# Kernel optimization log

Hardware: AMD Instinct MI355X
Metric: run time of the kernel (lower is better)

The kernel has to match this reference:

```python
import jax, jax.numpy as jnp
import numpy as np

FACTOR = 16
B = 65536
H = 50  # userids history length (mean-pooled)
# (name, vocab, factor_multiplier) in concat order of feature()
FEATS = [
    ("ip1", 256, 8), ("ip2", 256, 8), ("ip3", 256, 8),
    ("url", 2, 1), ("aurl", 2, 1),
    ("regionid", 35, 6), ("cityid", 370, 9), ("adexchange", 9, 4),
    ("adslotw", 21, 5), ("adsloth", 14, 4), ("adslotv", 7, 3),
    ("adslotfp", 275, 9), ("creativeid", 57, 6),
    ("bidprice", 2, 1), ("payprice", 295, 9), ("userids", 69, 7),
]


def setup_inputs() -> dict:
    key = jax.random.key(0)
    inp = {}
    for i, (name, vocab, mult) in enumerate(FEATS):
        k1, k2 = jax.random.split(jax.random.fold_in(key, i))
        shape = (B, H) if name == "userids" else (B,)
        inp["idx_" + name] = jax.random.randint(k1, shape, 0, vocab, dtype=jnp.int32)
        inp["E_" + name] = jax.random.normal(k2, (vocab, FACTOR * mult), dtype=jnp.float32) * 0.1
    dims = [FACTOR * 89, FACTOR * 64, FACTOR * 32, FACTOR * 16, 2]
    for i in range(4):
        k1, _ = jax.random.split(jax.random.fold_in(key, 100 + i))
        inp[f"W{i+1}"] = jax.random.normal(k1, (dims[i], dims[i + 1]), dtype=jnp.float32) * 0.02
        inp[f"b{i+1}"] = jnp.zeros((dims[i + 1],), dtype=jnp.float32)
    return inp


def reference(idx_ip1, idx_ip2, idx_ip3, idx_url, idx_aurl, idx_regionid,
              idx_cityid, idx_adexchange, idx_adslotw, idx_adsloth, idx_adslotv,
              idx_adslotfp, idx_creativeid, idx_bidprice, idx_payprice, idx_userids,
              E_ip1, E_ip2, E_ip3, E_url, E_aurl, E_regionid,
              E_cityid, E_adexchange, E_adslotw, E_adsloth, E_adslotv,
              E_adslotfp, E_creativeid, E_bidprice, E_payprice, E_userids,
              W1, b1, W2, b2, W3, b3, W4, b4):
    # 15 single-index gathers + mean-pooled userids, concatenated -> [B, factor*89]
    parts = [
        E_ip1[idx_ip1], E_ip2[idx_ip2], E_ip3[idx_ip3],
        E_url[idx_url], E_aurl[idx_aurl],
        E_regionid[idx_regionid], E_cityid[idx_cityid], E_adexchange[idx_adexchange],
        E_adslotw[idx_adslotw], E_adsloth[idx_adsloth], E_adslotv[idx_adslotv],
        E_adslotfp[idx_adslotfp], E_creativeid[idx_creativeid],
        E_bidprice[idx_bidprice], E_payprice[idx_payprice],
        E_userids[idx_userids].mean(axis=1),  # [B, H, d] -> [B, d]
    ]
    x = jnp.concatenate(parts, axis=-1)
    for W, b in ((W1, b1), (W2, b2), (W3, b3), (W4, b4)):
        x = jax.nn.relu(x @ W + b)  # ReLU after every layer, incl. last (as in source)
    return jax.nn.softmax(x, axis=-1)
```

## Files before the change

### kernel.cpp

```cpp
#include <hip/hip_runtime.h>
#include <stdint.h>

typedef unsigned short u16;
typedef __attribute__((ext_vector_type(8))) __bf16 bf16x8;
typedef __attribute__((ext_vector_type(4))) float f32x4;

#define B_TOTAL 65536
#define KPAD1   1440

__device__ __forceinline__ u16 f2bf(float f) {
  union { float f; uint32_t u; } v; v.f = f;
  uint32_t r = v.u + 0x7fffu + ((v.u >> 16) & 1u);
  return (u16)(r >> 16);
}

__device__ __forceinline__ void gload16(const void* g, void* lds) {
  __builtin_amdgcn_global_load_lds(
      (const __attribute__((address_space(1))) uint32_t*)g,
      (__attribute__((address_space(3))) uint32_t*)lds, 16, 0, 0);
}

constexpr int FDIM[15] = {128,128,128,16,16,96,144,64,80,64,48,144,96,16,144};
__device__ __constant__ int FOFF2[17] = {0,128,256,384,400,416,512,656,720,800,
                                         864,912,1056,1152,1168,1312,1440};
__device__ __constant__ int EOFF[15] = {0,32768,65536,98304,98336,98368,101728,
                                        155008,155584,157264,158160,158496,
                                        198096,203568,203600};
__device__ __constant__ int FDIMd[15] = {128,128,128,16,16,96,144,64,80,64,48,144,96,16,144};
#define EBF_TOTAL 246080

__global__ void wprep_kernel(const float* __restrict__ W, u16* __restrict__ Wt,
                             int K, int N, int Kpad) {
  int o = blockIdx.x * 256 + threadIdx.x;
  if (o >= N * Kpad) return;
  int k = o % Kpad;
  int n = o / Kpad;
  float v = (k < K) ? W[(size_t)k * N + n] : 0.0f;
  Wt[o] = f2bf(v);
}

struct EcvtArgs { const float* E[15]; };
__global__ void ecvt_kernel(EcvtArgs p, u16* __restrict__ ebf) {
  int i = blockIdx.x * 256 + threadIdx.x;
  if (i >= EBF_TOTAL) return;
  int f = 0;
#pragma unroll
  for (int t = 1; t < 15; ++t) if (i >= EOFF[t]) f = t;
  ebf[i] = f2bf(p.E[f][i - EOFF[f]]);
}

__global__ __launch_bounds__(512) void pool_kernel(const int* __restrict__ idx_u,
                                                   const float* __restrict__ E_u,
                                                   u16* __restrict__ P, int row_base) {
  __shared__ float eu_t[69 * 112];
  const int tid = threadIdx.x;
  {
    const float4* s4 = reinterpret_cast<const float4*>(E_u);
    float4* d4 = reinterpret_cast<float4*>(eu_t);
    for (int i = tid; i < 69 * 28; i += 512) d4[i] = s4[i];
  }
  const int lane = tid & 63;
  const int wv   = tid >> 6;
  const int row0 = blockIdx.x * 16 + wv * 2;

  const int* iu0 = idx_u + (size_t)(row_base + row0) * 50;
  const int myid0 = (lane < 50) ? iu0[lane] : 0;
  const int myid1 = (lane < 50) ? iu0[50 + lane] : 0;
  __syncthreads();

  const int half = lane >> 5;
  const int c    = lane & 31;

  auto POOL = [&](int myid, u16* prow) {
    float4 s = {0.f, 0.f, 0.f, 0.f};
    if (c < 28) {
      const float* eu = eu_t + c * 4;
      const int j0 = half * 25;
#pragma unroll
      for (int jb = 0; jb < 25; jb += 5) {
        float4 v0, v1, v2, v3, v4;
        {
          const int i0 = __shfl(myid, j0 + jb + 0);
          const int i1 = __shfl(myid, j0 + jb + 1);
          const int i2 = __shfl(myid, j0 + jb + 2);
          const int i3 = __shfl(myid, j0 + jb + 3);
          const int i4 = __shfl(myid, j0 + jb + 4);
          v0 = *reinterpret_cast<const float4*>(eu + i0 * 112);
          v1 = *reinterpret_cast<const float4*>(eu + i1 * 112);
          v2 = *reinterpret_cast<const float4*>(eu + i2 * 112);
          v3 = *reinterpret_cast<const float4*>(eu + i3 * 112);
          v4 = *reinterpret_cast<const float4*>(eu + i4 * 112);
        }
        s.x += v0.x + v1.x + v2.x + v3.x + v4.x;
        s.y += v0.y + v1.y + v2.y + v3.y + v4.y;
        s.z += v0.z + v1.z + v2.z + v3.z + v4.z;
        s.w += v0.w + v1.w + v2.w + v3.w + v4.w;
      }
      s.x += __shfl_xor(s.x, 32);
      s.y += __shfl_xor(s.y, 32);
      s.z += __shfl_xor(s.z, 32);
      s.w += __shfl_xor(s.w, 32);
      if (half == 0) {
        const float inv = 1.0f / 50.0f;
        ushort4 o;
        o.x = f2bf(s.x * inv);
        o.y = f2bf(s.y * inv);
        o.z = f2bf(s.z * inv);
        o.w = f2bf(s.w * inv);
        *reinterpret_cast<ushort4*>(prow + c * 4) = o;
      }
    } else if (half == 1) {
      ushort4 z; z.x = 0; z.y = 0; z.z = 0; z.w = 0;
      *reinterpret_cast<ushort4*>(prow + 112 + (c - 28) * 4) = z;
    }
  };

  POOL(myid0, P + (size_t)row0 * 128);
  POOL(myid1, P + (size_t)(row0 + 1) * 128);
}

#define TILE_ELE 16384

struct G1Args { const int* idx[15]; };

__global__ __launch_bounds__(512, 2) void gemm1g(
    G1Args p, const u16* __restrict__ ebf, const u16* __restrict__ P,
    const u16* __restrict__ Wt, const float* __restrict__ bias,
    u16* __restrict__ C, int N, int gm) {
  constexpr int K = KPAD1;
  constexpr int NT = K / 32;
  extern __shared__ __align__(16) u16 lds[];
  uint32_t* desc32 = reinterpret_cast<uint32_t*>(&lds[49152]);
  int* idxl = reinterpret_cast<int*>(&lds[49152 + 1440]);
  const int tid  = threadIdx.x;
  const int w    = tid >> 6;
  const int lane = tid & 63;
  const int fr   = lane & 15;
  const int kg   = lane >> 4;
  const int wm   = w >> 2;
  const int wn   = w & 3;

  const int nwg = gridDim.x;
  const int q = nwg >> 3, r = nwg & 7;
  const int xcd = blockIdx.x & 7, lid = blockIdx.x >> 3;
  const int swz = (xcd < r) ? (xcd * (q + 1) + lid) : (r * (q + 1) + (xcd - r) * q + lid);
  const int gn = N >> 8;
  const int bn = swz % gn, bm = swz / gn;
  const int rowBase = bm * 256, colBase = bn * 256;

  if (tid < 180) {
    const int c0 = tid * 8;
    int f = 0;
#pragma unroll
    for (int t = 1; t < 16; ++t) if (c0 >= FOFF2[t]) f = t;
    const u16* base = (f < 15) ? (ebf + EOFF[f]) : P;
    const int dim = (f < 15) ? FDIMd[f] : 128;
    const int off = c0 - FOFF2[f];
    desc32[tid * 4 + 0] = (uint32_t)(uintptr_t)base;
    desc32[tid * 4 + 1] = (uint32_t)((uintptr_t)base >> 32);
    desc32[tid * 4 + 2] = (uint32_t)dim;
    desc32[tid * 4 + 3] = (uint32_t)(off | (f << 16));
  }
#pragma unroll
  for (int f = 0; f < 15; ++f)
    if (tid < 256) idxl[tid * 17 + f] = p.idx[f][rowBase + tid];
  if (tid < 256) idxl[tid * 17 + 15] = tid;
  __syncthreads();

  const int srow  = lane >> 2;
  const int sslot = (lane & 3) ^ ((lane >> 3) & 3);
  const u16* Bsrc0 = Wt + (size_t)(colBase + w * 16 + srow) * K + sslot * 8;
  const size_t rstep = (size_t)128 * K;
  const int r0 = w * 16 + srow;

  f32x4 acc[8][4];
#pragma unroll
  for (int m = 0; m < 8; ++m)
#pragma unroll
    for (int n = 0; n < 4; ++n)
      acc[m][n] = f32x4{0.f, 0.f, 0.f, 0.f};

  const int aslot8 = (kg ^ ((fr >> 1) & 3)) * 8;
  const int ardA = (wm * 128 + fr) * 32 + aslot8;
  const int ardB = (wn * 64 + fr) * 32 + aslot8 + 8192;

  auto stageA = [&](int ldsElemBase, int kt) {
    const int g = kt * 4 + sslot;
    const uint32_t d0 = desc32[g * 4 + 0];
    const uint32_t d1 = desc32[g * 4 + 1];
    const uint32_t d2 = desc32[g * 4 + 2];
    const uint32_t d3 = desc32[g * 4 + 3];
    const u16* base = (const u16*)(((uint64_t)d1 << 32) | (uint64_t)d0);
    const int dim = (int)d2;
    const int off = (int)(d3 & 0xffffu);
    const int fid = (int)(d3 >> 16);
    const int i0 = idxl[r0 * 17 + fid];
    const int i1 = idxl[(r0 + 128) * 17 + fid];
    gload16(base + (size_t)i0 * dim + off, &lds[ldsElemBase + w * 512]);
    gload16(base + (size_t)i1 * dim + off, &lds[ldsElemBase + w * 512 + 4096]);
  };
  auto stageB = [&](int ldsElemBase, int kt) {
    const u16* s = Bsrc0 + (size_t)kt * 32;
    gload16(s,         &lds[ldsElemBase + w * 512]);
    gload16(s + rstep, &lds[ldsElemBase + w * 512 + 4096]);
  };

  stageA(0 * TILE_ELE,        0);
  stageB(0 * TILE_ELE + 8192, 0);
  stageA(1 * TILE_ELE,        1);
  stageB(1 * TILE_ELE + 8192, 1);

  for (int t = 0; t < NT; ++t) {
    const int cb = t % 3;
    const int sb = (t + 2) % 3;
    const bool dost = (t + 2) < NT;
    const int cA = cb * TILE_ELE;

    __builtin_amdgcn_sched_barrier(0);
    if (t < NT - 1) asm volatile("s_waitcnt vmcnt(4)" ::: "memory");
    else            asm volatile("s_waitcnt vmcnt(0)" ::: "memory");
    __builtin_amdgcn_s_barrier();
    __builtin_amdgcn_sched_barrier(0);

    if (dost) {
      stageA(sb * TILE_ELE,        t + 2);
      stageB(sb * TILE_ELE + 8192, t + 2);
    }

    bf16x8 a0 = *(const bf16x8*)&lds[cA + ardA + 0 * 512];
    bf16x8 a1 = *(const bf16x8*)&lds[cA + ardA + 1 * 512];
    bf16x8 a2 = *(const bf16x8*)&lds[cA + ardA + 2 * 512];
    bf16x8 a3 = *(const bf16x8*)&lds[cA + ardA + 3 * 512];
    bf16x8 b0 = *(const bf16x8*)&lds[cA + ardB + 0 * 512];
    bf16x8 b1 = *(const bf16x8*)&lds[cA + ardB + 1 * 512];
    bf16x8 b2 = *(const bf16x8*)&lds[cA + ardB + 2 * 512];
    bf16x8 b3 = *(const bf16x8*)&lds[cA + ardB + 3 * 512];
    bf16x8 c0 = *(const bf16x8*)&lds[cA + ardA + 2048 + 0 * 512];
    bf16x8 c1 = *(const bf16x8*)&lds[cA + ardA + 2048 + 1 * 512];
    bf16x8 c2 = *(const bf16x8*)&lds[cA + ardA + 2048 + 2 * 512];
    bf16x8 c3 = *(const bf16x8*)&lds[cA + ardA + 2048 + 3 * 512];
#pragma unroll
    for (int n = 0; n < 4; ++n) {
      bf16x8 bf = (n == 0) ? b0 : (n == 1) ? b1 : (n == 2) ? b2 : b3;
      acc[0][n] = __builtin_amdgcn_mfma_f32_16x16x32_bf16(bf, a0, acc[0][n], 0, 0, 0);
      acc[1][n] = __builtin_amdgcn_mfma_f32_16x16x32_bf16(bf, a1, acc[1][n], 0, 0, 0);
      acc[2][n] = __builtin_amdgcn_mfma_f32_16x16x32_bf16(bf, a2, acc[2][n], 0, 0, 0);
      acc[3][n] = __builtin_amdgcn_mfma_f32_16x16x32_bf16(bf, a3, acc[3][n], 0, 0, 0);
      acc[4][n] = __builtin_amdgcn_mfma_f32_16x16x32_bf16(bf, c0, acc[4][n], 0, 0, 0);
      acc[5][n] = __builtin_amdgcn_mfma_f32_16x16x32_bf16(bf, c1, acc[5][n], 0, 0, 0);
      acc[6][n] = __builtin_amdgcn_mfma_f32_16x16x32_bf16(bf, c2, acc[6][n], 0, 0, 0);
      acc[7][n] = __builtin_amdgcn_mfma_f32_16x16x32_bf16(bf, c3, acc[7][n], 0, 0, 0);
    }
  }

#pragma unroll
  for (int mm = 0; mm < 8; ++mm) {
    const int row = rowBase + wm * 128 + (mm >> 2) * 64 + (mm & 3) * 16 + fr;
#pragma unroll
    for (int n = 0; n < 4; ++n) {
      const int col0 = colBase + wn * 64 + n * 16 + kg * 4;
      ushort4 o;
      o.x = f2bf(fmaxf(acc[mm][n][0] + bias[col0 + 0], 0.f));
      o.y = f2bf(fmaxf(acc[mm][n][1] + bias[col0 + 1], 0.f));
      o.z = f2bf(fmaxf(acc[mm][n][2] + bias[col0 + 2], 0.f));
      o.w = f2bf(fmaxf(acc[mm][n][3] + bias[col0 + 3], 0.f));
      *reinterpret_cast<ushort4*>(&C[(size_t)row * N + col0]) = o;
    }
  }
}

__global__ __launch_bounds__(512, 2) void gemm8(
    const u16* __restrict__ A, const u16* __restrict__ Wt,
    const float* __restrict__ bias, u16* __restrict__ C,
    int M, int N, int K, int gm) {
  extern __shared__ __align__(16) u16 lds[];
  const int tid  = threadIdx.x;
  const int w    = tid >> 6;
  const int lane = tid & 63;
  const int fr   = lane & 15;
  const int kg   = lane >> 4;
  const int wm   = w >> 2;
  const int wn   = w & 3;

  const int nwg = gridDim.x;
  const int q = nwg >> 3, r = nwg & 7;
  const int xcd = blockIdx.x & 7, lid = blockIdx.x >> 3;
  const int swz = (xcd < r) ? (xcd * (q + 1) + lid) : (r * (q + 1) + (xcd - r) * q + lid);
  const int gn = N >> 8;
  const int bn = swz % gn, bm = swz / gn;
  const int rowBase = bm * 256, colBase = bn * 256;

  const int srow  = lane >> 2;
  const int sslot = (lane & 3) ^ ((lane >> 3) & 3);
  const u16* Asrc0 = A  + (size_t)(rowBase + w * 16 + srow) * K + sslot * 8;
  const u16* Bsrc0 = Wt + (size_t)(colBase + w * 16 + srow) * K + sslot * 8;
  const size_t rstep = (size_t)128 * K;

  const int NT = K / 32;

  f32x4 acc[8][4];
#pragma unroll
  for (int m = 0; m < 8; ++m)
#pragma unroll
    for (int n = 0; n < 4; ++n)
      acc[m][n] = f32x4{0.f, 0.f, 0.f, 0.f};

  const int aslot8 = (kg ^ ((fr >> 1) & 3)) * 8;
  const int ardA = (wm * 128 + fr) * 32 + aslot8;
  const int ardB = (wn * 64 + fr) * 32 + aslot8 + 8192;

  auto stage = [&](const u16* src0, int ldsElemBase, int kt) {
    const u16* s = src0 + (size_t)kt * 32;
    gload16(s,         &lds[ldsElemBase + w * 512]);
    gload16(s + rstep, &lds[ldsElemBase + w * 512 + 4096]);
  };

  stage(Asrc0, 0 * TILE_ELE,        0);
  stage(Bsrc0, 0 * TILE_ELE + 8192, 0);
  stage(Asrc0, 1 * TILE_ELE,        1);
  stage(Bsrc0, 1 * TILE_ELE + 8192, 1);

  for (int t = 0; t < NT; ++t) {
    const int cb = t % 3;
    const int sb = (t + 2) % 3;
    const bool dost = (t + 2) < NT;
    const int cA = cb * TILE_ELE;

    __builtin_amdgcn_sched_barrier(0);
    if (t < NT - 1) asm volatile("s_waitcnt vmcnt(4)" ::: "memory");
    else            asm volatile("s_waitcnt vmcnt(0)" ::: "memory");
    __builtin_amdgcn_s_barrier();
    __builtin_amdgcn_sched_barrier(0);

    bf16x8 a0 = *(const bf16x8*)&lds[cA + ardA + 0 * 512];
    bf16x8 a1 = *(const bf16x8*)&lds[cA + ardA + 1 * 512];
    bf16x8 a2 = *(const bf16x8*)&lds[cA + ardA + 2 * 512];
    bf16x8 a3 = *(const bf16x8*)&lds[cA + ardA + 3 * 512];
    bf16x8 b0 = *(const bf16x8*)&lds[cA + ardB + 0 * 512];
    bf16x8 b1 = *(const bf16x8*)&lds[cA + ardB + 1 * 512];
    bf16x8 b2 = *(const bf16x8*)&lds[cA + ardB + 2 * 512];
    bf16x8 b3 = *(const bf16x8*)&lds[cA + ardB + 3 * 512];
    bf16x8 c0 = *(const bf16x8*)&lds[cA + ardA + 2048 + 0 * 512];
    bf16x8 c1 = *(const bf16x8*)&lds[cA + ardA + 2048 + 1 * 512];
    bf16x8 c2 = *(const bf16x8*)&lds[cA + ardA + 2048 + 2 * 512];
    bf16x8 c3 = *(const bf16x8*)&lds[cA + ardA + 2048 + 3 * 512];
    if (dost) {
      stage(Asrc0, sb * TILE_ELE,        t + 2);
      stage(Bsrc0, sb * TILE_ELE + 8192, t + 2);
    }
#pragma unroll
    for (int n = 0; n < 4; ++n) {
      bf16x8 bf = (n == 0) ? b0 : (n == 1) ? b1 : (n == 2) ? b2 : b3;
      acc[0][n] = __builtin_amdgcn_mfma_f32_16x16x32_bf16(bf, a0, acc[0][n], 0, 0, 0);
      acc[1][n] = __builtin_amdgcn_mfma_f32_16x16x32_bf16(bf, a1, acc[1][n], 0, 0, 0);
      acc[2][n] = __builtin_amdgcn_mfma_f32_16x16x32_bf16(bf, a2, acc[2][n], 0, 0, 0);
      acc[3][n] = __builtin_amdgcn_mfma_f32_16x16x32_bf16(bf, a3, acc[3][n], 0, 0, 0);
      acc[4][n] = __builtin_amdgcn_mfma_f32_16x16x32_bf16(bf, c0, acc[4][n], 0, 0, 0);
      acc[5][n] = __builtin_amdgcn_mfma_f32_16x16x32_bf16(bf, c1, acc[5][n], 0, 0, 0);
      acc[6][n] = __builtin_amdgcn_mfma_f32_16x16x32_bf16(bf, c2, acc[6][n], 0, 0, 0);
      acc[7][n] = __builtin_amdgcn_mfma_f32_16x16x32_bf16(bf, c3, acc[7][n], 0, 0, 0);
    }
  }

#pragma unroll
  for (int mm = 0; mm < 8; ++mm) {
    const int row = rowBase + wm * 128 + (mm >> 2) * 64 + (mm & 3) * 16 + fr;
#pragma unroll
    for (int n = 0; n < 4; ++n) {
      const int col0 = colBase + wn * 64 + n * 16 + kg * 4;
      ushort4 o;
      o.x = f2bf(fmaxf(acc[mm][n][0] + bias[col0 + 0], 0.f));
      o.y = f2bf(fmaxf(acc[mm][n][1] + bias[col0 + 1], 0.f));
      o.z = f2bf(fmaxf(acc[mm][n][2] + bias[col0 + 2], 0.f));
      o.w = f2bf(fmaxf(acc[mm][n][3] + bias[col0 + 3], 0.f));
      *reinterpret_cast<ushort4*>(&C[(size_t)row * N + col0]) = o;
    }
  }
}

__global__ __launch_bounds__(512, 2) void gemm3f(
    const u16* __restrict__ A, const u16* __restrict__ Wt,
    const float* __restrict__ bias, const float* __restrict__ W4,
    const float* __restrict__ b4, float* __restrict__ out, int gm) {
  constexpr int K = 512, NT = 16;
  __shared__ __align__(16) u16 lds[2][12288];
  __shared__ float w4s[512];
  __shared__ float zred[4][128][2];
  const int tid  = threadIdx.x;
  const int w    = tid >> 6;
  const int lane = tid & 63;
  const int fr   = lane & 15;
  const int kg   = lane >> 4;
  const int wm   = w >> 2;
  const int wn   = w & 3;

  const int nwg = gridDim.x;
  const int q = nwg >> 3, r = nwg & 7;
  const int xcd = blockIdx.x & 7, lid = blockIdx.x >> 3;
  const int swz = (xcd < r) ? (xcd * (q + 1) + lid) : (r * (q + 1) + (xcd - r) * q + lid);
  const int rowBase = swz * 128;

  if (tid < 512) w4s[tid] = W4[tid];

  const int xslot = (tid & 3) ^ ((tid >> 3) & 3);
  const u16* Asrc  = A  + (size_t)(rowBase + (tid >> 2)) * K + xslot * 8;
  const u16* Bsrc0 = Wt + (size_t)(tid >> 2) * K + xslot * 8;
  const u16* Bsrc1 = Wt + (size_t)((tid >> 2) + 128) * K + xslot * 8;

  auto stage = [&](int buf, int kt) {
    const int ko = kt * 32;
    gload16(Asrc  + ko, &lds[buf][tid * 8]);
    gload16(Bsrc0 + ko, &lds[buf][4096 + tid * 8]);
    gload16(Bsrc1 + ko, &lds[buf][8192 + tid * 8]);
  };

  f32x4 acc[4][4];
#pragma unroll
  for (int m = 0; m < 4; ++m)
#pragma unroll
    for (int n = 0; n < 4; ++n)
      acc[m][n] = f32x4{0.f, 0.f, 0.f, 0.f};

  const int aslot8 = (kg ^ ((fr >> 1) & 3)) * 8;
  const int ardA = (wm * 64 + fr) * 32 + aslot8;
  const int ardB = 4096 + (wn * 64 + fr) * 32 + aslot8;

  stage(0, 0);
  stage(1, 1);

  for (int t = 0; t < NT; ++t) {
    const int cb = t & 1;
    if (t < NT - 1) asm volatile("s_waitcnt vmcnt(3)" ::: "memory");
    else            asm volatile("s_waitcnt vmcnt(0)" ::: "memory");
    __builtin_amdgcn_s_barrier();

    bf16x8 a0 = *(const bf16x8*)&lds[cb][ardA + 0 * 512];
    bf16x8 a1 = *(const bf16x8*)&lds[cb][ardA + 1 * 512];
    bf16x8 a2 = *(const bf16x8*)&lds[cb][ardA + 2 * 512];
    bf16x8 a3 = *(const bf16x8*)&lds[cb][ardA + 3 * 512];
    bf16x8 b0 = *(const bf16x8*)&lds[cb][ardB + 0 * 512];
    bf16x8 b1 = *(const bf16x8*)&lds[cb][ardB + 1 * 512];
    bf16x8 b2 = *(const bf16x8*)&lds[cb][ardB + 2 * 512];
    bf16x8 b3 = *(const bf16x8*)&lds[cb][ardB + 3 * 512];
    asm volatile("s_waitcnt lgkmcnt(0)" ::: "memory");
    __builtin_amdgcn_s_barrier();
    if (t + 2 < NT) stage(cb, t + 2);
    __builtin_amdgcn_sched_barrier(0);
    __builtin_amdgcn_s_setprio(1);
#pragma unroll
    for (int n = 0; n < 4; ++n) {
      bf16x8 bf = (n == 0) ? b0 : (n == 1) ? b1 : (n == 2) ? b2 : b3;
      acc[0][n] = __builtin_amdgcn_mfma_f32_16x16x32_bf16(bf, a0, acc[0][n], 0, 0, 0);
      acc[1][n] = __builtin_amdgcn_mfma_f32_16x16x32_bf16(bf, a1, acc[1][n], 0, 0, 0);
      acc[2][n] = __builtin_amdgcn_mfma_f32_16x16x32_bf16(bf, a2, acc[2][n], 0, 0, 0);
      acc[3][n] = __builtin_amdgcn_mfma_f32_16x16x32_bf16(bf, a3, acc[3][n], 0, 0, 0);
    }
    __builtin_amdgcn_s_setprio(0);
  }

  float z0[4] = {0.f, 0.f, 0.f, 0.f};
  float z1[4] = {0.f, 0.f, 0.f, 0.f};
#pragma unroll
  for (int n = 0; n < 4; ++n) {
    const int col0 = wn * 64 + n * 16 + kg * 4;
#pragma unroll
    for (int j = 0; j < 4; ++j) {
      const int c = col0 + j;
      const float bv = bias[c];
      const float w40 = w4s[c * 2];
      const float w41 = w4s[c * 2 + 1];
#pragma unroll
      for (int m = 0; m < 4; ++m) {
        const float h = fmaxf(acc[m][n][j] + bv, 0.f);
        z0[m] += h * w40;
        z1[m] += h * w41;
      }
    }
  }
#pragma unroll
  for (int m = 0; m < 4; ++m) {
    z0[m] += __shfl_xor(z0[m], 16); z0[m] += __shfl_xor(z0[m], 32);
    z1[m] += __shfl_xor(z1[m], 16); z1[m] += __shfl_xor(z1[m], 32);
  }
  if (kg == 0) {
#pragma unroll
    for (int m = 0; m < 4; ++m) {
      const int rr = wm * 64 + m * 16 + fr;
      zred[wn][rr][0] = z0[m];
      zred[wn][rr][1] = z1[m];
    }
  }
  __syncthreads();
  if (tid < 128) {
    const float s0 = zred[0][tid][0] + zred[1][tid][0] + zred[2][tid][0] + zred[3][tid][0];
    const float s1 = zred[0][tid][1] + zred[1][tid][1] + zred[2][tid][1] + zred[3][tid][1];
    const float zz0 = fmaxf(s0 + b4[0], 0.f);
    const float zz1 = fmaxf(s1 + b4[1], 0.f);
    const float mx = fmaxf(zz0, zz1);
    const float e0 = __expf(zz0 - mx), e1 = __expf(zz1 - mx);
    const float inv = 1.0f / (e0 + e1);
    out[(size_t)(rowBase + tid) * 2]     = e0 * inv;
    out[(size_t)(rowBase + tid) * 2 + 1] = e1 * inv;
  }
}

extern "C" void kernel_launch(void* const* d_in, const int* in_sizes, int n_in,
                              void* d_out, int out_size, void* d_ws, size_t ws_size,
                              hipStream_t stream) {
  const float* W1 = (const float*)d_in[32];
  const float* b1 = (const float*)d_in[33];
  const float* W2 = (const float*)d_in[34];
  const float* b2 = (const float*)d_in[35];
  const float* W3 = (const float*)d_in[36];
  const float* b3 = (const float*)d_in[37];
  const float* W4 = (const float*)d_in[38];
  const float* b4 = (const float*)d_in[39];

  (void)hipFuncSetAttribute(reinterpret_cast<const void*>(&gemm8),
                            hipFuncAttributeMaxDynamicSharedMemorySize, 98304);
  (void)hipFuncSetAttribute(reinterpret_cast<const void*>(&gemm1g),
                            hipFuncAttributeMaxDynamicSharedMemorySize, 118784);

  char* ws = (char*)d_ws;
  size_t off = 0;
  auto alloc = [&](size_t bytes) -> void* {
    void* p = ws + off;
    off += (bytes + 255) & ~(size_t)255;
    return p;
  };

  u16* W1t = (u16*)alloc((size_t)1024 * KPAD1 * 2);
  u16* W2t = (u16*)alloc((size_t)512 * 1024 * 2);
  u16* W3t = (u16*)alloc((size_t)256 * 512 * 2);
  u16* ebf = (u16*)alloc((size_t)EBF_TOTAL * 2);
  const size_t fixed = off;

  int nc = 64;
  const int cands[7] = {1, 2, 4, 8, 16, 32, 64};
  for (int ci = 0; ci < 7; ++ci) {
    size_t Bc = (size_t)B_TOTAL / cands[ci];
    size_t need = fixed + Bc * (128 + 1024 + 512) * 2 + 4096;
    if (need <= ws_size) { nc = cands[ci]; break; }
  }
  const int Bc = B_TOTAL / nc;

  u16* P  = (u16*)alloc((size_t)Bc * 128 * 2);
  u16* H1 = (u16*)alloc((size_t)Bc * 1024 * 2);
  u16* H2 = (u16*)alloc((size_t)Bc * 512 * 2);

  wprep_kernel<<<(1024 * KPAD1 + 255) / 256, 256, 0, stream>>>(W1, W1t, 1424, 1024, KPAD1);
  wprep_kernel<<<(512 * 1024 + 255) / 256, 256, 0, stream>>>(W2, W2t, 1024, 512, 1024);
  wprep_kernel<<<(256 * 512 + 255) / 256, 256, 0, stream>>>(W3, W3t, 512, 256, 512);

  EcvtArgs ea;
  for (int f = 0; f < 15; ++f) ea.E[f] = (const float*)d_in[2 * f + 1];
  ecvt_kernel<<<(EBF_TOTAL + 255) / 256, 256, 0, stream>>>(ea, ebf);

  G1Args g1;
  for (int f = 0; f < 15; ++f) g1.idx[f] = (const int*)d_in[2 * f];
  const int* idx_u = (const int*)d_in[30];
  const float* E_u = (const float*)d_in[31];

  const int gm = Bc / 256;
  for (int c = 0; c < nc; ++c) {
    G1Args g1c = g1;
    for (int f = 0; f < 15; ++f) g1c.idx[f] = g1.idx[f] + c * Bc;
    pool_kernel<<<Bc / 16, 512, 0, stream>>>(idx_u, E_u, P, c * Bc);
    gemm1g<<<gm * (1024 / 256), 512, 118784, stream>>>(g1c, ebf, P, W1t, b1, H1, 1024, gm);
    gemm8<<<gm * (512 / 256), 512, 98304, stream>>>(H1, W2t, b2, H2, Bc, 512, 1024, gm);
    gemm3f<<<Bc / 128, 512, 0, stream>>>(H2, W3t, b3, W4, b4,
                                         (float*)d_out + (size_t)c * Bc * 2, Bc / 128);
  }
}
```

Baseline: 366.7 us.

## Fold small-vocab embeddings into precomputed E·W1 tables to shrink GEMM1 K

Precomputes, for eight small-vocabulary features, the product of each embedding table with its slice of W1 into a 92x1024 table T. GEMM1 then runs over only the remaining large features (K drops from 1440 to 1056), and the epilogue adds the eight gathered T rows per output element. This cuts MFMA work and A-tile gathering in the largest GEMM. In exchange it adds a small prep kernel and extra scattered global reads in the epilogue, and rounds the folded contributions to bf16 separately from the main sum.

```diff
diff --git a/kernel.cpp b/kernel.cpp
--- a/kernel.cpp
+++ b/kernel.cpp
@@ -6,13 +6,17 @@
 typedef __attribute__((ext_vector_type(4))) float f32x4;
 
 #define B_TOTAL 65536
-#define KPAD1   1440
+#define KF1     1056
 
 __device__ __forceinline__ u16 f2bf(float f) {
   union { float f; uint32_t u; } v; v.f = f;
   uint32_t r = v.u + 0x7fffu + ((v.u >> 16) & 1u);
   return (u16)(r >> 16);
 }
+__device__ __forceinline__ float bf2f(u16 h) {
+  union { uint32_t u; float f; } v; v.u = ((uint32_t)h) << 16;
+  return v.f;
+}
 
 __device__ __forceinline__ void gload16(const void* g, void* lds) {
   __builtin_amdgcn_global_load_lds(
@@ -20,14 +24,18 @@
       (__attribute__((address_space(3))) uint32_t*)lds, 16, 0, 0);
 }
 
-constexpr int FDIM[15] = {128,128,128,16,16,96,144,64,80,64,48,144,96,16,144};
-__device__ __constant__ int FOFF2[17] = {0,128,256,384,400,416,512,656,720,800,
-                                         864,912,1056,1152,1168,1312,1440};
+__device__ __constant__ int NEWOFF[9] = {0,128,256,384,528,672,768,912,1056};
+__device__ __constant__ int SEGFID[8] = {0,1,2,6,11,12,14,15};
+__device__ __constant__ int SOLDX[8]  = {0,128,256,512,912,1056,1168,1312};
 __device__ __constant__ int EOFF[15] = {0,32768,65536,98304,98336,98368,101728,
                                         155008,155584,157264,158160,158496,
                                         198096,203568,203600};
 __device__ __constant__ int FDIMd[15] = {128,128,128,16,16,96,144,64,80,64,48,144,96,16,144};
 #define EBF_TOTAL 246080
+__device__ __constant__ int TROWc[8] = {0,2,4,39,48,69,83,90};
+__device__ __constant__ int TDIMc[8] = {16,16,96,64,80,64,48,16};
+__device__ __constant__ int TOLDX[8] = {384,400,416,656,720,800,864,1152};
+__device__ __constant__ int FOLDF[8] = {3,4,5,7,8,9,10,13};
 
 __global__ void wprep_kernel(const float* __restrict__ W, u16* __restrict__ Wt,
                              int K, int N, int Kpad) {
@@ -39,6 +47,20 @@
   Wt[o] = f2bf(v);
 }
 
+__global__ void wprep1_kernel(const float* __restrict__ W1, u16* __restrict__ Wt) {
+  int o = blockIdx.x * 256 + threadIdx.x;
+  if (o >= 1024 * KF1) return;
+  int k = o % KF1;
+  int n = o / KF1;
+  int s = 0;
+#pragma unroll
+  for (int t = 1; t < 8; ++t) if (k >= NEWOFF[t]) s = t;
+  const int loc = k - NEWOFF[s];
+  float v = 0.0f;
+  if (s < 7 || loc < 112) v = W1[(size_t)(SOLDX[s] + loc) * 1024 + n];
+  Wt[o] = f2bf(v);
+}
+
 struct EcvtArgs { const float* E[15]; };
 __global__ void ecvt_kernel(EcvtArgs p, u16* __restrict__ ebf) {
   int i = blockIdx.x * 256 + threadIdx.x;
@@ -47,6 +69,24 @@
 #pragma unroll
   for (int t = 1; t < 15; ++t) if (i >= EOFF[t]) f = t;
   ebf[i] = f2bf(p.E[f][i - EOFF[f]]);
+}
+
+struct TprepArgs { const float* E[8]; };
+__global__ void tprep_kernel(TprepArgs p, const float* __restrict__ W1,
+                             u16* __restrict__ T) {
+  int o = blockIdx.x * 256 + threadIdx.x;
+  if (o >= 92 * 1024) return;
+  const int n = o & 1023, rr = o >> 10;
+  int g = 0;
+#pragma unroll
+  for (int t = 1; t < 8; ++t) if (rr >= TROWc[t]) g = t;
+  const int v = rr - TROWc[g];
+  const int dim = TDIMc[g];
+  const float* e = p.E[g] + (size_t)v * dim;
+  const float* w = W1 + (size_t)TOLDX[g] * 1024 + n;
+  float s = 0.f;
+  for (int d = 0; d < dim; ++d) s += e[d] * w[(size_t)d * 1024];
+  T[o] = f2bf(s);
 }
 
 __global__ __launch_bounds__(512) void pool_kernel(const int* __restrict__ idx_u,
@@ -72,8 +112,8 @@
   const int c    = lane & 31;
 
   auto POOL = [&](int myid, u16* prow) {
-    float4 s = {0.f, 0.f, 0.f, 0.f};
     if (c < 28) {
+      float4 s = {0.f, 0.f, 0.f, 0.f};
       const float* eu = eu_t + c * 4;
       const int j0 = half * 25;
 #pragma unroll
@@ -109,14 +149,14 @@
         o.w = f2bf(s.w * inv);
         *reinterpret_cast<ushort4*>(prow + c * 4) = o;
       }
-    } else if (half == 1) {
+    } else {
       ushort4 z; z.x = 0; z.y = 0; z.z = 0; z.w = 0;
-      *reinterpret_cast<ushort4*>(prow + 112 + (c - 28) * 4) = z;
+      *reinterpret_cast<ushort4*>(prow + 112 + half * 16 + (c - 28) * 4) = z;
     }
   };
 
-  POOL(myid0, P + (size_t)row0 * 128);
-  POOL(myid1, P + (size_t)(row0 + 1) * 128);
+  POOL(myid0, P + (size_t)row0 * 144);
+  POOL(myid1, P + (size_t)(row0 + 1) * 144);
 }
 
 #define TILE_ELE 16384
@@ -125,13 +165,13 @@
 
 __global__ __launch_bounds__(512, 2) void gemm1g(
     G1Args p, const u16* __restrict__ ebf, const u16* __restrict__ P,
-    const u16* __restrict__ Wt, const float* __restrict__ bias,
-    u16* __restrict__ C, int N, int gm) {
-  constexpr int K = KPAD1;
+    const u16* __restrict__ T, const u16* __restrict__ Wt,
+    const float* __restrict__ bias, u16* __restrict__ C, int N, int gm) {
+  constexpr int K = KF1;
   constexpr int NT = K / 32;
   extern __shared__ __align__(16) u16 lds[];
   uint32_t* desc32 = reinterpret_cast<uint32_t*>(&lds[49152]);
-  int* idxl = reinterpret_cast<int*>(&lds[49152 + 1440]);
+  int* idxl = reinterpret_cast<int*>(&lds[49152 + 1056]);
   const int tid  = threadIdx.x;
   const int w    = tid >> 6;
   const int lane = tid & 63;
@@ -148,18 +188,19 @@
   const int bn = swz % gn, bm = swz / gn;
   const int rowBase = bm * 256, colBase = bn * 256;
 
-  if (tid < 180) {
+  if (tid < 132) {
     const int c0 = tid * 8;
-    int f = 0;
-#pragma unroll
-    for (int t = 1; t < 16; ++t) if (c0 >= FOFF2[t]) f = t;
-    const u16* base = (f < 15) ? (ebf + EOFF[f]) : P;
-    const int dim = (f < 15) ? FDIMd[f] : 128;
-    const int off = c0 - FOFF2[f];
+    int s = 0;
+#pragma unroll
+    for (int t = 1; t < 8; ++t) if (c0 >= NEWOFF[t]) s = t;
+    const int fid = SEGFID[s];
+    const u16* base = (fid < 15) ? (ebf + EOFF[fid]) : P;
+    const int dim = (fid < 15) ? FDIMd[fid] : 144;
+    const int off = c0 - NEWOFF[s];
     desc32[tid * 4 + 0] = (uint32_t)(uintptr_t)base;
     desc32[tid * 4 + 1] = (uint32_t)((uintptr_t)base >> 32);
     desc32[tid * 4 + 2] = (uint32_t)dim;
-    desc32[tid * 4 + 3] = (uint32_t)(off | (f << 16));
+    desc32[tid * 4 + 3] = (uint32_t)(off | (fid << 16));
   }
 #pragma unroll
   for (int f = 0; f < 15; ++f)
@@ -255,15 +296,26 @@
 
 #pragma unroll
   for (int mm = 0; mm < 8; ++mm) {
-    const int row = rowBase + wm * 128 + (mm >> 2) * 64 + (mm & 3) * 16 + fr;
+    const int rl  = wm * 128 + (mm >> 2) * 64 + (mm & 3) * 16 + fr;
+    const int row = rowBase + rl;
+    int tr[8];
+#pragma unroll
+    for (int g = 0; g < 8; ++g)
+      tr[g] = (TROWc[g] + idxl[rl * 17 + FOLDF[g]]) << 10;
 #pragma unroll
     for (int n = 0; n < 4; ++n) {
       const int col0 = colBase + wn * 64 + n * 16 + kg * 4;
+      float s0 = 0.f, s1 = 0.f, s2 = 0.f, s3 = 0.f;
+#pragma unroll
+      for (int g = 0; g < 8; ++g) {
+        const ushort4 tv = *reinterpret_cast<const ushort4*>(&T[tr[g] + col0]);
+        s0 += bf2f(tv.x); s1 += bf2f(tv.y); s2 += bf2f(tv.z); s3 += bf2f(tv.w);
+      }
       ushort4 o;
-      o.x = f2bf(fmaxf(acc[mm][n][0] + bias[col0 + 0], 0.f));
-      o.y = f2bf(fmaxf(acc[mm][n][1] + bias[col0 + 1], 0.f));
-      o.z = f2bf(fmaxf(acc[mm][n][2] + bias[col0 + 2], 0.f));
-      o.w = f2bf(fmaxf(acc[mm][n][3] + bias[col0 + 3], 0.f));
+      o.x = f2bf(fmaxf(acc[mm][n][0] + bias[col0 + 0] + s0, 0.f));
+      o.y = f2bf(fmaxf(acc[mm][n][1] + bias[col0 + 1] + s1, 0.f));
+      o.z = f2bf(fmaxf(acc[mm][n][2] + bias[col0 + 2] + s2, 0.f));
+      o.w = f2bf(fmaxf(acc[mm][n][3] + bias[col0 + 3] + s3, 0.f));
       *reinterpret_cast<ushort4*>(&C[(size_t)row * N + col0]) = o;
     }
   }
@@ -519,7 +571,7 @@
   (void)hipFuncSetAttribute(reinterpret_cast<const void*>(&gemm8),
                             hipFuncAttributeMaxDynamicSharedMemorySize, 98304);
   (void)hipFuncSetAttribute(reinterpret_cast<const void*>(&gemm1g),
-                            hipFuncAttributeMaxDynamicSharedMemorySize, 118784);
+                            hipFuncAttributeMaxDynamicSharedMemorySize, 117824);
 
   char* ws = (char*)d_ws;
   size_t off = 0;
@@ -529,32 +581,40 @@
     return p;
   };
 
-  u16* W1t = (u16*)alloc((size_t)1024 * KPAD1 * 2);
+  u16* W1t = (u16*)alloc((size_t)1024 * KF1 * 2);
   u16* W2t = (u16*)alloc((size_t)512 * 1024 * 2);
   u16* W3t = (u16*)alloc((size_t)256 * 512 * 2);
   u16* ebf = (u16*)alloc((size_t)EBF_TOTAL * 2);
+  u16* T   = (u16*)alloc((size_t)92 * 1024 * 2);
   const size_t fixed = off;
 
   int nc = 64;
   const int cands[7] = {1, 2, 4, 8, 16, 32, 64};
   for (int ci = 0; ci < 7; ++ci) {
     size_t Bc = (size_t)B_TOTAL / cands[ci];
-    size_t need = fixed + Bc * (128 + 1024 + 512) * 2 + 4096;
+    size_t need = fixed + Bc * (144 + 1024 + 512) * 2 + 4096;
     if (need <= ws_size) { nc = cands[ci]; break; }
   }
   const int Bc = B_TOTAL / nc;
 
-  u16* P  = (u16*)alloc((size_t)Bc * 128 * 2);
+  u16* P  = (u16*)alloc((size_t)Bc * 144 * 2);
   u16* H1 = (u16*)alloc((size_t)Bc * 1024 * 2);
   u16* H2 = (u16*)alloc((size_t)Bc * 512 * 2);
 
-  wprep_kernel<<<(1024 * KPAD1 + 255) / 256, 256, 0, stream>>>(W1, W1t, 1424, 1024, KPAD1);
+  wprep1_kernel<<<(1024 * KF1 + 255) / 256, 256, 0, stream>>>(W1, W1t);
   wprep_kernel<<<(512 * 1024 + 255) / 256, 256, 0, stream>>>(W2, W2t, 1024, 512, 1024);
   wprep_kernel<<<(256 * 512 + 255) / 256, 256, 0, stream>>>(W3, W3t, 512, 256, 512);
 
   EcvtArgs ea;
   for (int f = 0; f < 15; ++f) ea.E[f] = (const float*)d_in[2 * f + 1];
   ecvt_kernel<<<(EBF_TOTAL + 255) / 256, 256, 0, stream>>>(ea, ebf);
+
+  TprepArgs ta;
+  {
+    const int foldf[8] = {3, 4, 5, 7, 8, 9, 10, 13};
+    for (int g = 0; g < 8; ++g) ta.E[g] = (const float*)d_in[2 * foldf[g] + 1];
+  }
+  tprep_kernel<<<(92 * 1024 + 255) / 256, 256, 0, stream>>>(ta, W1, T);
 
   G1Args g1;
   for (int f = 0; f < 15; ++f) g1.idx[f] = (const int*)d_in[2 * f];
@@ -566,7 +626,7 @@
     G1Args g1c = g1;
     for (int f = 0; f < 15; ++f) g1c.idx[f] = g1.idx[f] + c * Bc;
     pool_kernel<<<Bc / 16, 512, 0, stream>>>(idx_u, E_u, P, c * Bc);
-    gemm1g<<<gm * (1024 / 256), 512, 118784, stream>>>(g1c, ebf, P, W1t, b1, H1, 1024, gm);
+    gemm1g<<<gm * (1024 / 256), 512, 117824, stream>>>(g1c, ebf, P, T, W1t, b1, H1, 1024, gm);
     gemm8<<<gm * (512 / 256), 512, 98304, stream>>>(H1, W2t, b2, H2, Bc, 512, 1024, gm);
     gemm3f<<<Bc / 128, 512, 0, stream>>>(H2, W3t, b3, W4, b4,
                                          (float*)d_out + (size_t)c * Bc * 2, Bc / 128);
```

Result: slower. 521.6 us (+42.2%).
